# Kernel optimization log

Hardware: AMD Instinct MI355X
Metric: run time of the kernel (lower is better)

## Reference

```python
import jax, jax.numpy as jnp
import numpy as np


def setup_inputs() -> dict:
    key = jax.random.key(0)
    n, d = 256, 64
    ks = jax.random.split(key, 8)
    x = jax.random.normal(ks[0], (n, d), jnp.float32)
    v = jax.random.normal(ks[1], (n, d), jnp.float32)
    # torch nn.Linear convention: weight shape (out_features, in_features)
    W1 = jax.random.normal(ks[2], (d, d), jnp.float32) * (1.0 / np.sqrt(d))
    b1 = jax.random.normal(ks[3], (d,), jnp.float32) * 0.1
    # W2 scaled small + b2 ~ scaled identity so g = M + M^T is well-conditioned (invertible)
    W2 = jax.random.normal(ks[4], (d * d, d), jnp.float32) * 0.02
    b2 = (3.0 * jnp.eye(d, dtype=jnp.float32)).reshape(d * d) \
         + jax.random.normal(ks[5], (d * d,), jnp.float32) * 0.01
    W3 = jax.random.normal(ks[6], (d, 2 * d), jnp.float32) * (1.0 / np.sqrt(2 * d))
    return {"t": 0, "x": x, "v": v, "W1": W1, "b1": b1, "W2": W2, "b2": b2, "W3": W3}


def reference(t, x, v, W1, b1, W2, b2, W3):
    # Connection_gnew.forward. t is unused (ODE-time placeholder), matching the original.
    n, d = x.shape
    # g network: linear1 -> tanh -> linear2 -> symmetrize
    h = jnp.tanh(x @ W1.T + b1)                      # (n, d)
    M = (h @ W2.T + b2).reshape(n, d, d)             # (n, d, d)
    g = M + jnp.transpose(M, (0, 2, 1))              # symmetric metric (n, d, d)
    g_inv = jnp.linalg.inv(g)
    # Analytic batch jacobian of g_flat wrt x (replaces autograd.functional.jacobian):
    # d M_flat[a]/d x[l] = sum_m W2[a,m] * (1 - h[m]^2) * W1[m,l]; then symmetrize (i<->j).
    s = 1.0 - h * h                                   # tanh' (n, d)
    J = jnp.einsum('am,nm,ml->nal', W2, s, W1).reshape(n, d, d, d)
    J = J + jnp.transpose(J, (0, 2, 1, 3))            # J[n,i,j,l] = d g_{ij} / d x_l
    # einsum('nkl,nijl,njil,nlij->nkij', g_inv, J, J, -J):
    # elementwise triple product over matching indices, then contract l with g_inv.
    T = J * jnp.transpose(J, (0, 2, 1, 3)) * (-jnp.transpose(J, (0, 2, 3, 1)))  # T[n,i,j,l]
    connection = 0.5 * jnp.einsum('nkl,nijl->nkij', g_inv, T)
    # dv[n,k] = -sum_{ij} v_i v_j connection[n,k,i,j]
    dv = -jnp.einsum('ni,nj,nkij->nk', v, v, connection)
    out = jnp.concatenate([v, dv], axis=-1) @ W3.T    # linear3, no bias
    return out
```

## Files before the change

### kernel.cpp

```cpp
#include <hip/hip_runtime.h>
#include <math.h>
#include <stdint.h>


typedef short short8 __attribute__((ext_vector_type(8)));
typedef float f32x4 __attribute__((ext_vector_type(4)));

__device__ __forceinline__ unsigned short f2bf(float f) {
  unsigned int u = __builtin_bit_cast(unsigned int, f);
  u += 0x7fffu + ((u >> 16) & 1u);
  return (unsigned short)(u >> 16);
}

__device__ __forceinline__ short8 as_short8(uint4 u) {
  union { uint4 a; short8 b; } cv; cv.a = u; return cv.b;
}

__global__ __launch_bounds__(256) void prep_w2s_kernel(const float* __restrict__ W2,
                                                       unsigned short* __restrict__ W2sB) {
  int idx = blockIdx.x * 256 + threadIdx.x;
  int i = idx >> 12, j = (idx >> 6) & 63, m = idx & 63;
  W2sB[idx] = f2bf(W2[(((i << 6) + j) << 6) + m] + W2[(((j << 6) + i) << 6) + m]);
}

__global__ __launch_bounds__(256, 1) void conn_kernel(
    const float* __restrict__ x, const float* __restrict__ v,
    const float* __restrict__ W1, const float* __restrict__ b1,
    const float* __restrict__ b2, const float* __restrict__ W3,
    const unsigned short* __restrict__ W2sB, float* __restrict__ out) {
  __shared__ __align__(16) unsigned short sKT[80 * 80];
  __shared__ __align__(16) float sg[64 * 68];
  __shared__ float spq[4][64];
  __shared__ __align__(16) float sh[64], sv[64], sx[64], sq[64], sz[64];

  const int n = blockIdx.x, t = threadIdx.x;
  const int wv = t >> 6, lane = t & 63, ln15 = lane & 15, quad = lane >> 4;

  if (t < 64) { sx[t] = x[(n << 6) + t]; sv[t] = v[(n << 6) + t]; }
  for (int e = t; e < 6400; e += 256) sKT[e] = 0;
  __syncthreads();

  if (t < 64) {
    float acc = b1[t];
    #pragma unroll 8
    for (int l = 0; l < 64; ++l) acc += sx[l] * W1[(t << 6) + l];
    sh[t] = tanhf(acc);
  }
  __syncthreads();

  for (int e = t; e < 4096; e += 256) {
    int m = e & 63, l = e >> 6;
    float hm = sh[m];
    sKT[l * 80 + m] = f2bf((1.f - hm * hm) * W1[(m << 6) + l]);
  }
  if (t < 64) sKT[64 * 80 + t] = f2bf(sh[t]);
  __syncthreads();

  short8 bf[5][2];
  #pragma unroll
  for (int tc = 0; tc < 5; ++tc)
    #pragma unroll
    for (int ks = 0; ks < 2; ++ks)
      bf[tc][ks] = *(const short8*)&sKT[(tc * 16 + ln15) * 80 + ks * 32 + quad * 8];

  f32x4 svj[4];
  #pragma unroll
  for (int tr = 0; tr < 4; ++tr) svj[tr] = *(const f32x4*)&sv[tr * 16 + quad * 4];

  float qacc[4] = {0.f, 0.f, 0.f, 0.f};

  const int foff = (ln15 << 6) + quad * 8;
  const unsigned short* sbase = W2sB + ((size_t)(16 * wv) << 12);

  uint4 af[4][2], afn[4][2];
  #pragma unroll
  for (int tc = 0; tc < 4; ++tc) {
    af[tc][0] = *(const uint4*)(sbase + (tc << 10) + foff);
    af[tc][1] = *(const uint4*)(sbase + (tc << 10) + foff + 32);
  }

  for (int ii = 0; ii < 16; ++ii) {
    const unsigned short* spn = W2sB + ((size_t)(16 * wv + ((ii + 1) & 15)) << 12);
    #pragma unroll
    for (int tc = 0; tc < 4; ++tc) {
      afn[tc][0] = *(const uint4*)(spn + (tc << 10) + foff);
      afn[tc][1] = *(const uint4*)(spn + (tc << 10) + foff + 32);
    }
    const int i = 16 * wv + ii;
    const float vi = sv[i];

    #pragma unroll
    for (int tr = 0; tr < 4; ++tr) {
      short8 a0 = as_short8(af[tr][0]), a1 = as_short8(af[tr][1]);
      f32x4 c1[4], c2[4], ce;
      #pragma unroll
      for (int tc = 0; tc < 4; ++tc) {
        f32x4 z4 = {0.f, 0.f, 0.f, 0.f};
        f32x4 u = __builtin_amdgcn_mfma_f32_16x16x32_bf16(a0, bf[tc][0], z4, 0, 0, 0);
        c1[tc]  = __builtin_amdgcn_mfma_f32_16x16x32_bf16(a1, bf[tc][1], u, 0, 0, 0);
        f32x4 w = __builtin_amdgcn_mfma_f32_16x16x32_bf16(bf[tr][0], as_short8(af[tc][0]), z4, 0, 0, 0);
        c2[tc]  = __builtin_amdgcn_mfma_f32_16x16x32_bf16(bf[tr][1], as_short8(af[tc][1]), w, 0, 0, 0);
      }
      {
        f32x4 z4 = {0.f, 0.f, 0.f, 0.f};
        f32x4 u = __builtin_amdgcn_mfma_f32_16x16x32_bf16(a0, bf[4][0], z4, 0, 0, 0);
        ce      = __builtin_amdgcn_mfma_f32_16x16x32_bf16(a1, bf[4][1], u, 0, 0, 0);
      }
      if (ln15 == 0)
        *(f32x4*)&sg[i * 68 + tr * 16 + quad * 4] = ce;

      #pragma unroll
      for (int tc = 0; tc < 4; ++tc) {
        float s = 0.f;
        #pragma unroll
        for (int r = 0; r < 4; ++r) {
          float a = c1[tc][r];
          s = fmaf(a * a * c2[tc][r], svj[tr][r], s);
        }
        qacc[tc] = fmaf(s, vi, qacc[tc]);
      }
    }
    #pragma unroll
    for (int tc = 0; tc < 4; ++tc) { af[tc][0] = afn[tc][0]; af[tc][1] = afn[tc][1]; }
  }

  #pragma unroll
  for (int tc = 0; tc < 4; ++tc) {
    float s = qacc[tc];
    s += __shfl_xor(s, 16, 64);
    s += __shfl_xor(s, 32, 64);
    if (quad == 0) spq[wv][tc * 16 + ln15] = s;
  }
  __syncthreads();

  for (int e = t; e < 4096; e += 256) {
    int r = e >> 6, c = e & 63;
    sg[r * 68 + c] += b2[(r << 6) + c] + b2[(c << 6) + r];
  }
  __syncthreads();

  if (t < 64) {
    float s = spq[0][t] + spq[1][t] + spq[2][t] + spq[3][t];
    sq[t] = s;
    sz[t] = s / sg[t * 68 + t];
  }
  __syncthreads();

  {
    const int r = 16 * wv + ln15;
    const float* grow = &sg[r * 68];
    const float dinv = 1.f / grow[r];
    const float qr = sq[r];
    for (int it = 0; it < 20; ++it) {
      float p = 0.f;
      #pragma unroll
      for (int cc = 0; cc < 16; ++cc) {
        int cidx = quad * 16 + cc;
        p += grow[cidx] * sz[cidx];
      }
      p += __shfl_xor(p, 16, 64);
      p += __shfl_xor(p, 32, 64);
      float zr = 0.f;
      if (quad == 0) zr = sz[r] + (qr - p) * dinv;
      __syncthreads();
      if (quad == 0) sz[r] = zr;
      __syncthreads();
    }
  }

  if (t < 64) {
    float accv = 0.f, accd = 0.f;
    #pragma unroll 8
    for (int c = 0; c < 64; ++c) {
      accv += sv[c] * W3[(t << 7) + c];
      accd += sz[c] * W3[(t << 7) + 64 + c];
    }
    out[(n << 6) + t] = accv + 0.5f * accd;
  }
}

extern "C" void kernel_launch(void* const* d_in, const int* in_sizes, int n_in,
                              void* d_out, int out_size, void* d_ws, size_t ws_size,
                              hipStream_t stream) {
  (void)in_sizes; (void)n_in; (void)out_size; (void)ws_size;
  const float* x  = (const float*)d_in[1];
  const float* v  = (const float*)d_in[2];
  const float* W1 = (const float*)d_in[3];
  const float* b1 = (const float*)d_in[4];
  const float* W2 = (const float*)d_in[5];
  const float* b2 = (const float*)d_in[6];
  const float* W3 = (const float*)d_in[7];
  unsigned short* W2sB = (unsigned short*)d_ws;

  hipLaunchKernelGGL(prep_w2s_kernel, dim3(1024), dim3(256), 0, stream, W2, W2sB);
  hipLaunchKernelGGL(conn_kernel, dim3(256), dim3(256), 0, stream,
                     x, v, W1, b1, b2, W3, W2sB, (float*)d_out);
}
```

Baseline: 102.8 us.

## Double block size to 8 waves and parallelise serial phases with shuffles

Raises the block from 4 to 8 waves, so each wave handles 8 rows of i instead of 16 in the MFMA main loop. The small matvecs (W1·x and W3 output) now use 8 lanes per output with float4 loads and shuffle reductions instead of 64 threads each running serial loops. The Jacobi iteration double-buffers z to save one barrier per iteration. The prep kernel is vectorised to process 8 elements per thread. The zeroing of sKT is cut down to the pad rows, and 512-thread blocks may raise register pressure under the new launch bounds.

```diff
diff --git a/kernel.cpp b/kernel.cpp
--- a/kernel.cpp
+++ b/kernel.cpp
@@ -18,37 +18,54 @@
 
 __global__ __launch_bounds__(256) void prep_w2s_kernel(const float* __restrict__ W2,
                                                        unsigned short* __restrict__ W2sB) {
-  int idx = blockIdx.x * 256 + threadIdx.x;
-  int i = idx >> 12, j = (idx >> 6) & 63, m = idx & 63;
-  W2sB[idx] = f2bf(W2[(((i << 6) + j) << 6) + m] + W2[(((j << 6) + i) << 6) + m]);
-}
-
-__global__ __launch_bounds__(256, 1) void conn_kernel(
+  int g = blockIdx.x * 256 + threadIdx.x;
+  int i = g >> 9, j = (g >> 3) & 63, m8 = (g & 7) << 3;
+  const float* pa = &W2[((((i << 6) + j) << 6) + m8)];
+  const float* pb = &W2[((((j << 6) + i) << 6) + m8)];
+  float4 a0 = *(const float4*)pa, a1 = *(const float4*)(pa + 4);
+  float4 b0 = *(const float4*)pb, b1 = *(const float4*)(pb + 4);
+  short8 r;
+  r[0] = (short)f2bf(a0.x + b0.x); r[1] = (short)f2bf(a0.y + b0.y);
+  r[2] = (short)f2bf(a0.z + b0.z); r[3] = (short)f2bf(a0.w + b0.w);
+  r[4] = (short)f2bf(a1.x + b1.x); r[5] = (short)f2bf(a1.y + b1.y);
+  r[6] = (short)f2bf(a1.z + b1.z); r[7] = (short)f2bf(a1.w + b1.w);
+  *(short8*)&W2sB[(size_t)g << 3] = r;
+}
+
+__global__ __launch_bounds__(512, 2) void conn_kernel(
     const float* __restrict__ x, const float* __restrict__ v,
     const float* __restrict__ W1, const float* __restrict__ b1,
     const float* __restrict__ b2, const float* __restrict__ W3,
     const unsigned short* __restrict__ W2sB, float* __restrict__ out) {
   __shared__ __align__(16) unsigned short sKT[80 * 80];
   __shared__ __align__(16) float sg[64 * 68];
-  __shared__ float spq[4][64];
-  __shared__ __align__(16) float sh[64], sv[64], sx[64], sq[64], sz[64];
+  __shared__ float spq[8][64];
+  __shared__ __align__(16) float sh[64], sv[64], sx[64], sq[64];
+  __shared__ __align__(16) float sz2[2][64];
 
   const int n = blockIdx.x, t = threadIdx.x;
   const int wv = t >> 6, lane = t & 63, ln15 = lane & 15, quad = lane >> 4;
-
-  if (t < 64) { sx[t] = x[(n << 6) + t]; sv[t] = v[(n << 6) + t]; }
-  for (int e = t; e < 6400; e += 256) sKT[e] = 0;
-  __syncthreads();
-
-  if (t < 64) {
-    float acc = b1[t];
-    #pragma unroll 8
-    for (int l = 0; l < 64; ++l) acc += sx[l] * W1[(t << 6) + l];
-    sh[t] = tanhf(acc);
-  }
-  __syncthreads();
-
-  for (int e = t; e < 4096; e += 256) {
+  const int o8 = t >> 3, s8 = t & 7;
+
+  if (t < 64) sx[t] = x[(n << 6) + t];
+  else if (t < 128) sv[t - 64] = v[(n << 6) + (t - 64)];
+  for (int e = t; e < 1280; e += 512) sKT[5120 + e] = 0;
+  __syncthreads();
+
+  {
+    const float* w1r = &W1[(o8 << 6) + (s8 << 3)];
+    float4 wa = *(const float4*)w1r, wb = *(const float4*)(w1r + 4);
+    float4 xa = *(const float4*)&sx[s8 << 3], xb = *(const float4*)&sx[(s8 << 3) + 4];
+    float acc = wa.x * xa.x + wa.y * xa.y + wa.z * xa.z + wa.w * xa.w
+              + wb.x * xb.x + wb.y * xb.y + wb.z * xb.z + wb.w * xb.w;
+    acc += __shfl_xor(acc, 1);
+    acc += __shfl_xor(acc, 2);
+    acc += __shfl_xor(acc, 4);
+    if (s8 == 0) sh[o8] = tanhf(acc + b1[o8]);
+  }
+  __syncthreads();
+
+  for (int e = t; e < 4096; e += 512) {
     int m = e & 63, l = e >> 6;
     float hm = sh[m];
     sKT[l * 80 + m] = f2bf((1.f - hm * hm) * W1[(m << 6) + l]);
@@ -70,7 +87,7 @@
   float qacc[4] = {0.f, 0.f, 0.f, 0.f};
 
   const int foff = (ln15 << 6) + quad * 8;
-  const unsigned short* sbase = W2sB + ((size_t)(16 * wv) << 12);
+  const unsigned short* sbase = W2sB + ((size_t)(8 * wv) << 12);
 
   uint4 af[4][2], afn[4][2];
   #pragma unroll
@@ -79,14 +96,14 @@
     af[tc][1] = *(const uint4*)(sbase + (tc << 10) + foff + 32);
   }
 
-  for (int ii = 0; ii < 16; ++ii) {
-    const unsigned short* spn = W2sB + ((size_t)(16 * wv + ((ii + 1) & 15)) << 12);
+  for (int ii = 0; ii < 8; ++ii) {
+    const unsigned short* spn = W2sB + ((size_t)(8 * wv + ((ii + 1) & 7)) << 12);
     #pragma unroll
     for (int tc = 0; tc < 4; ++tc) {
       afn[tc][0] = *(const uint4*)(spn + (tc << 10) + foff);
       afn[tc][1] = *(const uint4*)(spn + (tc << 10) + foff + 32);
     }
-    const int i = 16 * wv + ii;
+    const int i = 8 * wv + ii;
     const float vi = sv[i];
 
     #pragma unroll
@@ -133,49 +150,58 @@
   }
   __syncthreads();
 
-  for (int e = t; e < 4096; e += 256) {
+  for (int e = t; e < 4096; e += 512) {
     int r = e >> 6, c = e & 63;
     sg[r * 68 + c] += b2[(r << 6) + c] + b2[(c << 6) + r];
   }
   __syncthreads();
 
   if (t < 64) {
-    float s = spq[0][t] + spq[1][t] + spq[2][t] + spq[3][t];
+    float s = spq[0][t] + spq[1][t] + spq[2][t] + spq[3][t]
+            + spq[4][t] + spq[5][t] + spq[6][t] + spq[7][t];
     sq[t] = s;
-    sz[t] = s / sg[t * 68 + t];
+    sz2[0][t] = s / sg[t * 68 + t];
   }
   __syncthreads();
 
   {
-    const int r = 16 * wv + ln15;
-    const float* grow = &sg[r * 68];
-    const float dinv = 1.f / grow[r];
-    const float qr = sq[r];
+    const int row = o8;
+    const float* grow = &sg[row * 68];
+    const float dinv = 1.f / grow[row];
+    const float qr = sq[row];
+    int pb = 0;
     for (int it = 0; it < 20; ++it) {
       float p = 0.f;
       #pragma unroll
-      for (int cc = 0; cc < 16; ++cc) {
-        int cidx = quad * 16 + cc;
-        p += grow[cidx] * sz[cidx];
-      }
-      p += __shfl_xor(p, 16, 64);
-      p += __shfl_xor(p, 32, 64);
-      float zr = 0.f;
-      if (quad == 0) zr = sz[r] + (qr - p) * dinv;
+      for (int cc = 0; cc < 8; ++cc) {
+        int c = (cc << 3) + s8;
+        p += grow[c] * sz2[pb][c];
+      }
+      p += __shfl_xor(p, 1);
+      p += __shfl_xor(p, 2);
+      p += __shfl_xor(p, 4);
+      if (s8 == 0) sz2[pb ^ 1][row] = sz2[pb][row] + (qr - p) * dinv;
       __syncthreads();
-      if (quad == 0) sz[r] = zr;
-      __syncthreads();
+      pb ^= 1;
     }
   }
 
-  if (t < 64) {
-    float accv = 0.f, accd = 0.f;
-    #pragma unroll 8
-    for (int c = 0; c < 64; ++c) {
-      accv += sv[c] * W3[(t << 7) + c];
-      accd += sz[c] * W3[(t << 7) + 64 + c];
-    }
-    out[(n << 6) + t] = accv + 0.5f * accd;
+  {
+    const float* w3r = &W3[o8 << 7];
+    float4 wva = *(const float4*)&w3r[s8 << 3];
+    float4 wvb = *(const float4*)&w3r[(s8 << 3) + 4];
+    float4 wda = *(const float4*)&w3r[64 + (s8 << 3)];
+    float4 wdb = *(const float4*)&w3r[64 + (s8 << 3) + 4];
+    float4 va = *(const float4*)&sv[s8 << 3], vb = *(const float4*)&sv[(s8 << 3) + 4];
+    float4 za = *(const float4*)&sz2[0][s8 << 3], zb = *(const float4*)&sz2[0][(s8 << 3) + 4];
+    float acc = wva.x * va.x + wva.y * va.y + wva.z * va.z + wva.w * va.w
+              + wvb.x * vb.x + wvb.y * vb.y + wvb.z * vb.z + wvb.w * vb.w
+              + 0.5f * (wda.x * za.x + wda.y * za.y + wda.z * za.z + wda.w * za.w
+                      + wdb.x * zb.x + wdb.y * zb.y + wdb.z * zb.z + wdb.w * zb.w);
+    acc += __shfl_xor(acc, 1);
+    acc += __shfl_xor(acc, 2);
+    acc += __shfl_xor(acc, 4);
+    if (s8 == 0) out[(n << 6) + o8] = acc;
   }
 }
 
@@ -192,7 +218,7 @@
   const float* W3 = (const float*)d_in[7];
   unsigned short* W2sB = (unsigned short*)d_ws;
 
-  hipLaunchKernelGGL(prep_w2s_kernel, dim3(1024), dim3(256), 0, stream, W2, W2sB);
-  hipLaunchKernelGGL(conn_kernel, dim3(256), dim3(256), 0, stream,
+  hipLaunchKernelGGL(prep_w2s_kernel, dim3(128), dim3(256), 0, stream, W2, W2sB);
+  hipLaunchKernelGGL(conn_kernel, dim3(256), dim3(512), 0, stream,
                      x, v, W1, b1, b2, W3, W2sB, (float*)d_out);
 }
```

Result: slower. 105.8 us (+2.9%).
